# Kernel optimization log

Hardware: AMD Instinct MI355X
Metric: run time of the kernel (lower is better)

Reference implementation:

```python
import jax, jax.numpy as jnp
import numpy as np

B, S, C, H, W, SHIFT = 8, 4096, 512, 16, 64, 32
HD = C // H        # head dim = 32
NW = S // W        # num windows = 64
EPS = 1e-5


def setup_inputs() -> dict:
    key = jax.random.key(0)
    ks = jax.random.split(key, 8)
    def n(k, shape, s=0.02):
        return jax.random.normal(k, shape, jnp.float32) * s
    return {
        "x": jax.random.normal(ks[0], (B, S, C), jnp.float32),
        "norm1_g": jnp.ones((C,), jnp.float32),
        "norm1_b": jnp.zeros((C,), jnp.float32),
        "qkv_w": n(ks[1], (3 * C, C)),
        "qkv_b": jnp.zeros((3 * C,), jnp.float32),
        "rel_bias": n(ks[2], (2 * W - 1, H)),
        "proj_w": n(ks[3], (C, C)),
        "proj_b": jnp.zeros((C,), jnp.float32),
        "norm2_g": jnp.ones((C,), jnp.float32),
        "norm2_b": jnp.zeros((C,), jnp.float32),
        "fc1_w": n(ks[4], (4 * C, C)),
        "fc1_b": jnp.zeros((4 * C,), jnp.float32),
        "fc2_w": n(ks[5], (C, 4 * C)),
        "fc2_b": jnp.zeros((C,), jnp.float32),
    }


def _layernorm(x, g, b):
    m = x.mean(-1, keepdims=True)
    v = ((x - m) ** 2).mean(-1, keepdims=True)
    return (x - m) * jax.lax.rsqrt(v + EPS) * g + b


def _attn_mask():
    # shifted-window mask, (NW, W, W) of {0, -100}
    seg = np.zeros(S, np.float32)
    seg[S - W: S - SHIFT] = 1.0
    seg[S - SHIFT:] = 2.0
    mw = seg.reshape(NW, W)
    d = mw[:, None, :] - mw[:, :, None]
    return jnp.asarray(np.where(d != 0, -100.0, 0.0).astype(np.float32))


def reference(x, norm1_g, norm1_b, qkv_w, qkv_b, rel_bias, proj_w, proj_b,
              norm2_g, norm2_b, fc1_w, fc1_b, fc2_w, fc2_b):
    # ---- W-MSA branch ----
    h = _layernorm(x, norm1_g, norm1_b)
    h = jnp.roll(h, -SHIFT, axis=1)                    # cyclic shift
    xw = h.reshape(B * NW, W, C)                       # window partition
    qkv = (xw @ qkv_w.T + qkv_b).reshape(B * NW, W, 3, H, HD)
    q, k, v = qkv[:, :, 0], qkv[:, :, 1], qkv[:, :, 2]  # (B_, W, H, HD)
    scale = HD ** -0.5
    attn = jnp.einsum('bnhd,bmhd->bhnm', q * scale, k)  # (B_, H, W, W)
    # relative position bias (1D): index = i - j + W - 1
    idx = jnp.arange(W)[:, None] - jnp.arange(W)[None, :] + (W - 1)
    bias = rel_bias[idx].transpose(2, 0, 1)             # (H, W, W)
    attn = attn + bias[None]
    attn = attn.reshape(B, NW, H, W, W) + _attn_mask()[None, :, None]
    attn = jax.nn.softmax(attn.reshape(B * NW, H, W, W), axis=-1)
    o = jnp.einsum('bhnm,bmhd->bnhd', attn, v).reshape(B * NW, W, C)
    o = o @ proj_w.T + proj_b
    o = o.reshape(B, S, C)
    o = jnp.roll(o, SHIFT, axis=1)                     # reverse cyclic shift
    x1 = x + o                                         # residual (drop_path = identity)
    # ---- MLP branch ----
    h2 = _layernorm(x1, norm2_g, norm2_b)
    h2 = jax.nn.gelu(h2 @ fc1_w.T + fc1_b, approximate=False)
    return x1 + (h2 @ fc2_w.T + fc2_b)
```

## Files before the change

kernel.cpp:

```cpp
#include <hip/hip_runtime.h>
#include <hip/hip_bf16.h>

typedef short short8 __attribute__((ext_vector_type(8)));
typedef short short4v __attribute__((ext_vector_type(4)));
typedef float f32x4 __attribute__((ext_vector_type(4)));

#define SHIFT_ 32

__device__ __forceinline__ float bf2f(unsigned short u) {
    union { unsigned int i; float f; } z; z.i = ((unsigned)u) << 16; return z.f;
}
__device__ __forceinline__ unsigned short f2bf(float f) {
    union { float f; unsigned int i; } z; z.f = f;
    unsigned int x = z.i;
    x += 0x7fffu + ((x >> 16) & 1u);
    return (unsigned short)(x >> 16);
}

__global__ __launch_bounds__(256)
void f2bf_all(const float* __restrict__ s0, const float* __restrict__ s1,
              const float* __restrict__ s2, const float* __restrict__ s3,
              unsigned short* __restrict__ dst) {
    int b = blockIdx.x;
    const float* src; int off;
    if (b < 768)       { src = s0; off = b * 1024; }
    else if (b < 1024) { src = s1; off = (b - 768) * 1024; }
    else if (b < 2048) { src = s2; off = (b - 1024) * 1024; }
    else               { src = s3; off = (b - 2048) * 1024; }
    int i = off + threadIdx.x * 4;
    f32x4 v = *(const f32x4*)(src + i);
    short4v o;
#pragma unroll
    for (int j = 0; j < 4; j++) o[j] = (short)f2bf(v[j]);
    *(short4v*)(dst + (size_t)b * 1024 + threadIdx.x * 4) = o;
}

template <bool BF16IN>
__global__ __launch_bounds__(256)
void ln_kernel(const void* __restrict__ srcv,
               const float* __restrict__ gam,
               const float* __restrict__ bet,
               unsigned short* __restrict__ dst, int roll) {
    int wid = threadIdx.x >> 6, lane = threadIdx.x & 63;
    int m = (blockIdx.x << 2) + wid;
    int b = m >> 12, s = m & 4095;
    int ms = (b << 12) | ((s + roll) & 4095);
    float f[8], sum = 0.f, sq = 0.f;
    if (BF16IN) {
        short8 v = *(const short8*)((const unsigned short*)srcv + (size_t)ms * 512 + lane * 8);
#pragma unroll
        for (int j = 0; j < 8; j++) f[j] = bf2f((unsigned short)v[j]);
    } else {
        const float* p = (const float*)srcv + (size_t)ms * 512 + lane * 8;
        f32x4 v0 = *(const f32x4*)p;
        f32x4 v1 = *(const f32x4*)(p + 4);
#pragma unroll
        for (int j = 0; j < 4; j++) { f[j] = v0[j]; f[j + 4] = v1[j]; }
    }
#pragma unroll
    for (int j = 0; j < 8; j++) { sum += f[j]; sq += f[j] * f[j]; }
#pragma unroll
    for (int o = 1; o < 64; o <<= 1) { sum += __shfl_xor(sum, o); sq += __shfl_xor(sq, o); }
    float mean = sum * (1.f / 512.f);
    float rstd = rsqrtf(sq * (1.f / 512.f) - mean * mean + 1e-5f);
    const float* gp = gam + lane * 8;
    const float* bp = bet + lane * 8;
    f32x4 g0 = *(const f32x4*)gp, g1 = *(const f32x4*)(gp + 4);
    f32x4 b0 = *(const f32x4*)bp, b1 = *(const f32x4*)(bp + 4);
    short8 ov;
#pragma unroll
    for (int j = 0; j < 4; j++) {
        ov[j]     = (short)f2bf((f[j] - mean) * rstd * g0[j] + b0[j]);
        ov[j + 4] = (short)f2bf((f[j + 4] - mean) * rstd * g1[j] + b1[j]);
    }
    *(short8*)(dst + (size_t)m * 512 + lane * 8) = ov;
}

template <int N, int K, int EPI, bool OUTF32, bool RESBF16>
__global__ __launch_bounds__(256, 3)
void gemm_kernel(const unsigned short* __restrict__ A,
                 const unsigned short* __restrict__ Wt,
                 const float* __restrict__ bias,
                 void* __restrict__ outv,
                 const void* __restrict__ extra, int nwg) {
    __shared__ __attribute__((aligned(16))) unsigned short smem[24576];
    int cpx = nwg >> 3;
    int bid = (blockIdx.x & 7) * cpx + (blockIdx.x >> 3);
    const int nbx = N / 128;
    int bcol = bid % nbx, brow = bid / nbx;
    int m0 = brow << 7, n0 = bcol << 7;
    int t = threadIdx.x, lane = t & 63;
    int wr = (t >> 7) << 6;
    int wc = ((t >> 6) & 1) << 6;
    int rsel = lane & 15, qq = lane >> 4;
    int slotr = ((qq ^ (rsel & 3)) << 3);

    int r0 = t >> 2;
    int s0 = (((t & 3) ^ (r0 & 3)) << 3);
    int r1 = (t + 256) >> 2;
    int s1 = ((((t + 256) & 3) ^ (r1 & 3)) << 3);

#define SAb(b) (smem + (b) * 4096)
#define SBb(b) (smem + 12288 + (b) * 4096)
#define STAGE(buf, k0)                                                                  \
    do {                                                                                \
        __builtin_amdgcn_global_load_lds(                                               \
            (const __attribute__((address_space(1))) void*)(A + (size_t)(m0 + r0) * K + (k0) + s0), \
            (__attribute__((address_space(3))) void*)(SAb(buf) + t * 8), 16, 0, 0);     \
        __builtin_amdgcn_global_load_lds(                                               \
            (const __attribute__((address_space(1))) void*)(Wt + (size_t)(n0 + r0) * K + (k0) + s0), \
            (__attribute__((address_space(3))) void*)(SBb(buf) + t * 8), 16, 0, 0);     \
        __builtin_amdgcn_global_load_lds(                                               \
            (const __attribute__((address_space(1))) void*)(A + (size_t)(m0 + r1) * K + (k0) + s1), \
            (__attribute__((address_space(3))) void*)(SAb(buf) + (t + 256) * 8), 16, 0, 0); \
        __builtin_amdgcn_global_load_lds(                                               \
            (const __attribute__((address_space(1))) void*)(Wt + (size_t)(n0 + r1) * K + (k0) + s1), \
            (__attribute__((address_space(3))) void*)(SBb(buf) + (t + 256) * 8), 16, 0, 0); \
    } while (0)

    f32x4 zero4 = {0.f, 0.f, 0.f, 0.f};
    f32x4 acc[4][4];
#pragma unroll
    for (int mi = 0; mi < 4; mi++)
#pragma unroll
        for (int ni = 0; ni < 4; ni++) acc[mi][ni] = zero4;

    const int NT = K / 32;
    STAGE(0, 0);
    STAGE(1, 32);
    for (int tt = 0; tt < NT; tt++) {
        int cur = tt % 3;
        if (tt < NT - 1) asm volatile("s_waitcnt vmcnt(4)" ::: "memory");
        else             asm volatile("s_waitcnt vmcnt(0)" ::: "memory");
        __builtin_amdgcn_sched_barrier(0);
        __builtin_amdgcn_s_barrier();
        __builtin_amdgcn_sched_barrier(0);
        if (tt + 2 < NT) STAGE((tt + 2) % 3, (tt + 2) * 32);
        short8 af[4], bf4[4];
#pragma unroll
        for (int mi = 0; mi < 4; mi++)
            af[mi] = *(const short8*)(SAb(cur) + (wr + mi * 16 + rsel) * 32 + slotr);
#pragma unroll
        for (int ni = 0; ni < 4; ni++)
            bf4[ni] = *(const short8*)(SBb(cur) + (wc + ni * 16 + rsel) * 32 + slotr);
#pragma unroll
        for (int mi = 0; mi < 4; mi++)
#pragma unroll
            for (int ni = 0; ni < 4; ni++)
                acc[mi][ni] = __builtin_amdgcn_mfma_f32_16x16x32_bf16(af[mi], bf4[ni], acc[mi][ni], 0, 0, 0);
    }
    __builtin_amdgcn_s_barrier();
#undef STAGE

    int jbase = qq << 2;
    if (!OUTF32) {
        unsigned short* ep = smem + (t >> 6) * 4096;
#pragma unroll
        for (int ni = 0; ni < 4; ni++) {
            float bv = bias[n0 + wc + ni * 16 + rsel];
            int cswz = ((ni ^ qq) << 4) + rsel;
#pragma unroll
            for (int mi = 0; mi < 4; mi++)
#pragma unroll
                for (int j = 0; j < 4; j++) {
                    float v = acc[mi][ni][j] + bv;
                    if (EPI == 1) v = 0.5f * v * (1.f + erff(v * 0.70710678118654752f));
                    ep[(mi * 16 + jbase + j) * 64 + cswz] = f2bf(v);
                }
        }
        unsigned short* outp = (unsigned short*)outv;
#pragma unroll
        for (int it = 0; it < 8; it++) {
            int chunk = it * 64 + lane;
            int rr = chunk >> 3, c8 = (chunk & 7) << 3;
            int g = (rr >> 2) & 3;
            short8 vv = *(const short8*)(ep + rr * 64 + (c8 ^ (g << 4)));
            int grow = m0 + wr + rr, gcol = n0 + wc + c8;
            if (EPI == 2) {
                int orow = (grow & ~4095) | ((grow + SHIFT_) & 4095);
                const float* xr = (const float*)extra + (size_t)orow * N + gcol;
                f32x4 x0 = *(const f32x4*)xr, x1v = *(const f32x4*)(xr + 4);
                short8 ov;
#pragma unroll
                for (int e = 0; e < 4; e++) {
                    ov[e]     = (short)f2bf(bf2f((unsigned short)vv[e]) + x0[e]);
                    ov[e + 4] = (short)f2bf(bf2f((unsigned short)vv[e + 4]) + x1v[e]);
                }
                *(short8*)(outp + (size_t)orow * N + gcol) = ov;
            } else {
                *(short8*)(outp + (size_t)grow * N + gcol) = vv;
            }
        }
    } else {
#pragma unroll
        for (int ni = 0; ni < 4; ni++) {
            int gcol = n0 + wc + ni * 16 + rsel;
            float bv = bias[gcol];
#pragma unroll
            for (int mi = 0; mi < 4; mi++) {
#pragma unroll
                for (int j = 0; j < 4; j++) {
                    int grow = m0 + wr + mi * 16 + jbase + j;
                    float v = acc[mi][ni][j] + bv;
                    size_t oidx;
                    if (EPI == 2) {
                        int orow = (grow & ~4095) | ((grow + SHIFT_) & 4095);
                        oidx = (size_t)orow * N + gcol;
                        v += ((const float*)extra)[oidx];
                    } else {
                        oidx = (size_t)grow * N + gcol;
                        if (EPI == 3)
                            v += RESBF16 ? bf2f(((const unsigned short*)extra)[oidx])
                                         : ((const float*)extra)[oidx];
                    }
                    ((float*)outv)[oidx] = v;
                }
            }
        }
    }
#undef SAb
#undef SBb
}

__global__ __launch_bounds__(256, 2)
void attn_kernel(const unsigned short* __restrict__ qkv,
                 const float* __restrict__ relb,
                 unsigned short* __restrict__ obuf) {
    __shared__ __attribute__((aligned(16))) unsigned short Pl[4][64 * 72];
    __shared__ __attribute__((aligned(16))) unsigned short Vt[4][32 * 72];
    __shared__ float biasd[4][128];
    int t = threadIdx.x;
    int wid = t >> 6, lane = t & 63;
    int win = blockIdx.x >> 2;
    int h0 = (blockIdx.x & 3) << 2;
    int h = h0 + wid;
    const unsigned short* base = qkv + (size_t)win * 98304 + h * 32;

    float* bd = biasd[wid];
    bd[lane] = relb[lane * 16 + h];
    if (lane < 63) bd[lane + 64] = relb[(lane + 64) * 16 + h];

    int rsel = lane & 15, ksel = (lane >> 4) << 3;
    short8 qf[4], kf[4];
#pragma unroll
    for (int i = 0; i < 4; i++) {
        qf[i] = *(const short8*)(base + (size_t)(i * 16 + rsel) * 1536 + ksel);
        kf[i] = *(const short8*)(base + (size_t)(i * 16 + rsel) * 1536 + 512 + ksel);
    }
    f32x4 zero4 = {0.f, 0.f, 0.f, 0.f};
    f32x4 accS[4][4];
#pragma unroll
    for (int mi = 0; mi < 4; mi++)
#pragma unroll
        for (int ni = 0; ni < 4; ni++) accS[mi][ni] = zero4;
#pragma unroll
    for (int mi = 0; mi < 4; mi++)
#pragma unroll
        for (int ni = 0; ni < 4; ni++)
            accS[mi][ni] = __builtin_amdgcn_mfma_f32_16x16x32_bf16(qf[mi], kf[ni], accS[mi][ni], 0, 0, 0);

    unsigned short* vt = Vt[wid];
#pragma unroll 8
    for (int it = 0; it < 32; it++) {
        int idx = (it << 6) + lane;
        int vr = idx >> 5, vd = idx & 31;
        vt[vd * 72 + vr] = base[(size_t)vr * 1536 + 1024 + vd];
    }
    __syncthreads();

    const float scale = 0.17677669529663687f;
    bool masked = ((win & 63) == 63);
    int jbase = (lane >> 4) << 2;
    float rs[4][4];
#pragma unroll
    for (int mi = 0; mi < 4; mi++) {
#pragma unroll
        for (int ni = 0; ni < 4; ni++) {
            int colb = ni * 16 + rsel;
#pragma unroll
            for (int j = 0; j < 4; j++) {
                int row = mi * 16 + jbase + j;
                float v = accS[mi][ni][j] * scale + bd[row - colb + 63];
                if (masked && ((row < 32) != (colb < 32))) v -= 100.f;
                accS[mi][ni][j] = v;
            }
        }
#pragma unroll
        for (int j = 0; j < 4; j++) {
            float m = fmaxf(fmaxf(accS[mi][0][j], accS[mi][1][j]),
                            fmaxf(accS[mi][2][j], accS[mi][3][j]));
            m = fmaxf(m, __shfl_xor(m, 1));
            m = fmaxf(m, __shfl_xor(m, 2));
            m = fmaxf(m, __shfl_xor(m, 4));
            m = fmaxf(m, __shfl_xor(m, 8));
            float ssum = 0.f;
#pragma unroll
            for (int ni = 0; ni < 4; ni++) {
                float p = __expf(accS[mi][ni][j] - m);
                accS[mi][ni][j] = p; ssum += p;
            }
            ssum += __shfl_xor(ssum, 1);
            ssum += __shfl_xor(ssum, 2);
            ssum += __shfl_xor(ssum, 4);
            ssum += __shfl_xor(ssum, 8);
            rs[mi][j] = 1.f / ssum;
        }
    }
    unsigned short* pl = Pl[wid];
#pragma unroll
    for (int mi = 0; mi < 4; mi++)
#pragma unroll
        for (int ni = 0; ni < 4; ni++)
#pragma unroll
            for (int j = 0; j < 4; j++)
                pl[(mi * 16 + jbase + j) * 72 + ni * 16 + rsel] = f2bf(accS[mi][ni][j] * rs[mi][j]);
    __syncthreads();

    f32x4 accO[4][2];
#pragma unroll
    for (int mi = 0; mi < 4; mi++) { accO[mi][0] = zero4; accO[mi][1] = zero4; }
#pragma unroll
    for (int kk = 0; kk < 2; kk++) {
        short8 pa[4], vb[2];
#pragma unroll
        for (int mi = 0; mi < 4; mi++)
            pa[mi] = *(const short8*)(pl + (mi * 16 + rsel) * 72 + (kk << 5) + ksel);
#pragma unroll
        for (int ni = 0; ni < 2; ni++)
            vb[ni] = *(const short8*)(vt + (ni * 16 + rsel) * 72 + (kk << 5) + ksel);
#pragma unroll
        for (int mi = 0; mi < 4; mi++)
#pragma unroll
            for (int ni = 0; ni < 2; ni++)
                accO[mi][ni] = __builtin_amdgcn_mfma_f32_16x16x32_bf16(pa[mi], vb[ni], accO[mi][ni], 0, 0, 0);
    }
    __syncthreads();
    unsigned short* ot = (unsigned short*)Pl;
    int colb = wid * 32;
#pragma unroll
    for (int mi = 0; mi < 4; mi++)
#pragma unroll
        for (int ni = 0; ni < 2; ni++)
#pragma unroll
            for (int j = 0; j < 4; j++)
                ot[(mi * 16 + jbase + j) * 140 + colb + ni * 16 + rsel] = f2bf(accO[mi][ni][j]);
    __syncthreads();
    unsigned short* ob = obuf + (size_t)win * 32768 + h0 * 32;
#pragma unroll
    for (int it = 0; it < 4; it++) {
        int chunk = it * 256 + t;
        int row = chunk >> 4, c8 = (chunk & 15) << 3;
        short8 vv = *(const short8*)(ot + row * 140 + c8);
        *(short8*)(ob + (size_t)row * 512 + c8) = vv;
    }
}

extern "C" void kernel_launch(void* const* d_in, const int* in_sizes, int n_in,
                              void* d_out, int out_size, void* d_ws, size_t ws_size,
                              hipStream_t stream) {
    (void)in_sizes; (void)n_in; (void)out_size;
    const float* x       = (const float*)d_in[0];
    const float* norm1_g = (const float*)d_in[1];
    const float* norm1_b = (const float*)d_in[2];
    const float* qkv_w   = (const float*)d_in[3];
    const float* qkv_b   = (const float*)d_in[4];
    const float* rel_b   = (const float*)d_in[5];
    const float* proj_w  = (const float*)d_in[6];
    const float* proj_b  = (const float*)d_in[7];
    const float* norm2_g = (const float*)d_in[8];
    const float* norm2_b = (const float*)d_in[9];
    const float* fc1_w   = (const float*)d_in[10];
    const float* fc1_b   = (const float*)d_in[11];
    const float* fc2_w   = (const float*)d_in[12];
    const float* fc2_b   = (const float*)d_in[13];

    char* ws = (char*)d_ws;
    unsigned short* hn   = (unsigned short*)(ws);
    unsigned short* qkvb = (unsigned short*)(ws + 33554432);
    unsigned short* obuf = hn;
    unsigned short* wq   = (unsigned short*)(ws + 167772160);
    unsigned short* wp   = (unsigned short*)(ws + 167772160 + 1572864);
    unsigned short* w1   = (unsigned short*)(ws + 167772160 + 1572864 + 524288);
    unsigned short* w2   = (unsigned short*)(ws + 167772160 + 1572864 + 524288 + 2097152);
    unsigned short* x1b  = (unsigned short*)(ws + 174063616);
    float* x1f           = (float*)d_out;
    float* outf          = (float*)d_out;
    bool bf16x1 = ws_size >= 207618048ull;

    f2bf_all<<<3072, 256, 0, stream>>>(qkv_w, proj_w, fc1_w, fc2_w, wq);
    ln_kernel<false><<<8192, 256, 0, stream>>>(x, norm1_g, norm1_b, hn, SHIFT_);
    gemm_kernel<1536, 512, 0, false, false><<<3072, 256, 0, stream>>>(hn, wq, qkv_b, qkvb, nullptr, 3072);
    attn_kernel<<<2048, 256, 0, stream>>>(qkvb, rel_b, obuf);
    if (bf16x1) {
        gemm_kernel<512, 512, 2, false, false><<<1024, 256, 0, stream>>>(obuf, wp, proj_b, x1b, x, 1024);
        ln_kernel<true><<<8192, 256, 0, stream>>>(x1b, norm2_g, norm2_b, hn, 0);
        gemm_kernel<2048, 512, 1, false, false><<<4096, 256, 0, stream>>>(hn, w1, fc1_b, qkvb, nullptr, 4096);
        gemm_kernel<512, 2048, 3, true, true><<<1024, 256, 0, stream>>>(qkvb, w2, fc2_b, outf, x1b, 1024);
    } else {
        gemm_kernel<512, 512, 2, true, false><<<1024, 256, 0, stream>>>(obuf, wp, proj_b, x1f, x, 1024);
        ln_kernel<false><<<8192, 256, 0, stream>>>(x1f, norm2_g, norm2_b, hn, 0);
        gemm_kernel<2048, 512, 1, false, false><<<4096, 256, 0, stream>>>(hn, w1, fc1_b, qkvb, nullptr, 4096);
        gemm_kernel<512, 2048, 3, true, false><<<1024, 256, 0, stream>>>(qkvb, w2, fc2_b, outf, x1f, 1024);
    }
}
```

Measured before the change: 365.2 us.

## Enlarge GEMM block tile to 256x128 with 128x64 per-wave tiles

Each GEMM workgroup now computes a 256x128 output tile instead of 128x128: every wave holds 8x4 MFMA accumulators, and the triple-buffered LDS stages grow to fit twice as many A rows. The aim is to raise arithmetic intensity per LDS fragment load and per global load of B, and to halve the grid sizes. The cost is more registers and LDS per block, so launch bounds drop to 2 blocks per SM. Fewer workgroups also means coarser load balance across CUs.

Measured after the change: 380.6 us. 1.04x slower.

```diff
diff --git a/kernel.cpp b/kernel.cpp
--- a/kernel.cpp
+++ b/kernel.cpp
@@ -77,51 +77,50 @@
 }
 
 template <int N, int K, int EPI, bool OUTF32, bool RESBF16>
-__global__ __launch_bounds__(256, 3)
+__global__ __launch_bounds__(256, 2)
 void gemm_kernel(const unsigned short* __restrict__ A,
                  const unsigned short* __restrict__ Wt,
                  const float* __restrict__ bias,
                  void* __restrict__ outv,
                  const void* __restrict__ extra, int nwg) {
-    __shared__ __attribute__((aligned(16))) unsigned short smem[24576];
+    __shared__ __attribute__((aligned(16))) unsigned short smem[36864];
     int cpx = nwg >> 3;
     int bid = (blockIdx.x & 7) * cpx + (blockIdx.x >> 3);
     const int nbx = N / 128;
     int bcol = bid % nbx, brow = bid / nbx;
-    int m0 = brow << 7, n0 = bcol << 7;
-    int t = threadIdx.x, lane = t & 63;
-    int wr = (t >> 7) << 6;
-    int wc = ((t >> 6) & 1) << 6;
+    int m0 = brow << 8, n0 = bcol << 7;
+    int t = threadIdx.x, lane = t & 63, wid = t >> 6;
+    int wr = (wid >> 1) << 7;
+    int wc = (wid & 1) << 6;
     int rsel = lane & 15, qq = lane >> 4;
     int slotr = ((qq ^ (rsel & 3)) << 3);
 
-    int r0 = t >> 2;
-    int s0 = (((t & 3) ^ (r0 & 3)) << 3);
-    int r1 = (t + 256) >> 2;
-    int s1 = ((((t + 256) & 3) ^ (r1 & 3)) << 3);
-
-#define SAb(b) (smem + (b) * 4096)
-#define SBb(b) (smem + 12288 + (b) * 4096)
-#define STAGE(buf, k0)                                                                  \
-    do {                                                                                \
-        __builtin_amdgcn_global_load_lds(                                               \
-            (const __attribute__((address_space(1))) void*)(A + (size_t)(m0 + r0) * K + (k0) + s0), \
-            (__attribute__((address_space(3))) void*)(SAb(buf) + t * 8), 16, 0, 0);     \
-        __builtin_amdgcn_global_load_lds(                                               \
-            (const __attribute__((address_space(1))) void*)(Wt + (size_t)(n0 + r0) * K + (k0) + s0), \
-            (__attribute__((address_space(3))) void*)(SBb(buf) + t * 8), 16, 0, 0);     \
-        __builtin_amdgcn_global_load_lds(                                               \
-            (const __attribute__((address_space(1))) void*)(A + (size_t)(m0 + r1) * K + (k0) + s1), \
-            (__attribute__((address_space(3))) void*)(SAb(buf) + (t + 256) * 8), 16, 0, 0); \
-        __builtin_amdgcn_global_load_lds(                                               \
-            (const __attribute__((address_space(1))) void*)(Wt + (size_t)(n0 + r1) * K + (k0) + s1), \
-            (__attribute__((address_space(3))) void*)(SBb(buf) + (t + 256) * 8), 16, 0, 0); \
-    } while (0)
+    int ar[4], as_[4];
+#pragma unroll
+    for (int i = 0; i < 4; i++) {
+        int c = t + i * 256;
+        ar[i] = c >> 2;
+        as_[i] = (((c & 3) ^ ((c >> 2) & 3)) << 3);
+    }
+
+#define GLD(src, dst) __builtin_amdgcn_global_load_lds(                         \
+        (const __attribute__((address_space(1))) void*)(src),                  \
+        (__attribute__((address_space(3))) void*)(dst), 16, 0, 0)
+
+    auto STAGE = [&](int buf, int k0) {
+        unsigned short* base = smem + buf * 12288;
+#pragma unroll
+        for (int i = 0; i < 4; i++)
+            GLD(A + (size_t)(m0 + ar[i]) * K + k0 + as_[i], base + (t + i * 256) * 8);
+#pragma unroll
+        for (int i = 0; i < 2; i++)
+            GLD(Wt + (size_t)(n0 + ar[i]) * K + k0 + as_[i], base + 8192 + (t + i * 256) * 8);
+    };
 
     f32x4 zero4 = {0.f, 0.f, 0.f, 0.f};
-    f32x4 acc[4][4];
-#pragma unroll
-    for (int mi = 0; mi < 4; mi++)
+    f32x4 acc[8][4];
+#pragma unroll
+    for (int mi = 0; mi < 8; mi++)
 #pragma unroll
         for (int ni = 0; ni < 4; ni++) acc[mi][ni] = zero4;
 
@@ -130,37 +129,39 @@
     STAGE(1, 32);
     for (int tt = 0; tt < NT; tt++) {
         int cur = tt % 3;
-        if (tt < NT - 1) asm volatile("s_waitcnt vmcnt(4)" ::: "memory");
+        if (tt < NT - 1) asm volatile("s_waitcnt vmcnt(6)" ::: "memory");
         else             asm volatile("s_waitcnt vmcnt(0)" ::: "memory");
         __builtin_amdgcn_sched_barrier(0);
         __builtin_amdgcn_s_barrier();
         __builtin_amdgcn_sched_barrier(0);
         if (tt + 2 < NT) STAGE((tt + 2) % 3, (tt + 2) * 32);
-        short8 af[4], bf4[4];
-#pragma unroll
-        for (int mi = 0; mi < 4; mi++)
-            af[mi] = *(const short8*)(SAb(cur) + (wr + mi * 16 + rsel) * 32 + slotr);
+        const unsigned short* aB = smem + cur * 12288;
+        const unsigned short* bB = aB + 8192;
+        short8 af[8], bf4[4];
+#pragma unroll
+        for (int mi = 0; mi < 8; mi++)
+            af[mi] = *(const short8*)(aB + (wr + mi * 16 + rsel) * 32 + slotr);
 #pragma unroll
         for (int ni = 0; ni < 4; ni++)
-            bf4[ni] = *(const short8*)(SBb(cur) + (wc + ni * 16 + rsel) * 32 + slotr);
-#pragma unroll
-        for (int mi = 0; mi < 4; mi++)
+            bf4[ni] = *(const short8*)(bB + (wc + ni * 16 + rsel) * 32 + slotr);
+#pragma unroll
+        for (int mi = 0; mi < 8; mi++)
 #pragma unroll
             for (int ni = 0; ni < 4; ni++)
                 acc[mi][ni] = __builtin_amdgcn_mfma_f32_16x16x32_bf16(af[mi], bf4[ni], acc[mi][ni], 0, 0, 0);
     }
     __builtin_amdgcn_s_barrier();
-#undef STAGE
+#undef GLD
 
     int jbase = qq << 2;
     if (!OUTF32) {
-        unsigned short* ep = smem + (t >> 6) * 4096;
+        unsigned short* ep = smem + wid * 8192;
 #pragma unroll
         for (int ni = 0; ni < 4; ni++) {
             float bv = bias[n0 + wc + ni * 16 + rsel];
             int cswz = ((ni ^ qq) << 4) + rsel;
 #pragma unroll
-            for (int mi = 0; mi < 4; mi++)
+            for (int mi = 0; mi < 8; mi++)
 #pragma unroll
                 for (int j = 0; j < 4; j++) {
                     float v = acc[mi][ni][j] + bv;
@@ -170,7 +171,7 @@
         }
         unsigned short* outp = (unsigned short*)outv;
 #pragma unroll
-        for (int it = 0; it < 8; it++) {
+        for (int it = 0; it < 16; it++) {
             int chunk = it * 64 + lane;
             int rr = chunk >> 3, c8 = (chunk & 7) << 3;
             int g = (rr >> 2) & 3;
@@ -197,7 +198,7 @@
             int gcol = n0 + wc + ni * 16 + rsel;
             float bv = bias[gcol];
 #pragma unroll
-            for (int mi = 0; mi < 4; mi++) {
+            for (int mi = 0; mi < 8; mi++) {
 #pragma unroll
                 for (int j = 0; j < 4; j++) {
                     int grow = m0 + wr + mi * 16 + jbase + j;
@@ -218,8 +219,6 @@
             }
         }
     }
-#undef SAb
-#undef SBb
 }
 
 __global__ __launch_bounds__(256, 2)
@@ -389,17 +388,17 @@
 
     f2bf_all<<<3072, 256, 0, stream>>>(qkv_w, proj_w, fc1_w, fc2_w, wq);
     ln_kernel<false><<<8192, 256, 0, stream>>>(x, norm1_g, norm1_b, hn, SHIFT_);
-    gemm_kernel<1536, 512, 0, false, false><<<3072, 256, 0, stream>>>(hn, wq, qkv_b, qkvb, nullptr, 3072);
+    gemm_kernel<1536, 512, 0, false, false><<<1536, 256, 0, stream>>>(hn, wq, qkv_b, qkvb, nullptr, 1536);
     attn_kernel<<<2048, 256, 0, stream>>>(qkvb, rel_b, obuf);
     if (bf16x1) {
-        gemm_kernel<512, 512, 2, false, false><<<1024, 256, 0, stream>>>(obuf, wp, proj_b, x1b, x, 1024);
+        gemm_kernel<512, 512, 2, false, false><<<512, 256, 0, stream>>>(obuf, wp, proj_b, x1b, x, 512);
         ln_kernel<true><<<8192, 256, 0, stream>>>(x1b, norm2_g, norm2_b, hn, 0);
-        gemm_kernel<2048, 512, 1, false, false><<<4096, 256, 0, stream>>>(hn, w1, fc1_b, qkvb, nullptr, 4096);
-        gemm_kernel<512, 2048, 3, true, true><<<1024, 256, 0, stream>>>(qkvb, w2, fc2_b, outf, x1b, 1024);
+        gemm_kernel<2048, 512, 1, false, false><<<2048, 256, 0, stream>>>(hn, w1, fc1_b, qkvb, nullptr, 2048);
+        gemm_kernel<512, 2048, 3, true, true><<<512, 256, 0, stream>>>(qkvb, w2, fc2_b, outf, x1b, 512);
     } else {
-        gemm_kernel<512, 512, 2, true, false><<<1024, 256, 0, stream>>>(obuf, wp, proj_b, x1f, x, 1024);
+        gemm_kernel<512, 512, 2, true, false><<<512, 256, 0, stream>>>(obuf, wp, proj_b, x1f, x, 512);
         ln_kernel<false><<<8192, 256, 0, stream>>>(x1f, norm2_g, norm2_b, hn, 0);
-        gemm_kernel<2048, 512, 1, false, false><<<4096, 256, 0, stream>>>(hn, w1, fc1_b, qkvb, nullptr, 4096);
-        gemm_kernel<512, 2048, 3, true, false><<<1024, 256, 0, stream>>>(qkvb, w2, fc2_b, outf, x1f, 1024);
-    }
-}
+        gemm_kernel<2048, 512, 1, false, false><<<2048, 256, 0, stream>>>(hn, w1, fc1_b, qkvb, nullptr, 2048);
+        gemm_kernel<512, 2048, 3, true, false><<<512, 256, 0, stream>>>(qkvb, w2, fc2_b, outf, x1f, 512);
+    }
+}
```
